# Kernel optimization log

Measured on AMD Instinct MI355X. Metric: run time of the kernel, lower is better.

The kernel has to match this reference:

```python
import jax, jax.numpy as jnp
import numpy as np
import math

NATOM = 20000
NEIGH = 600000
NWAVE = 8
MAX_L = 3
CUTOFF = 5.0
EMB_NL = [16, 16]
J_SEQ = [[1, 1, 0], [1, 1, 2], [2, 2, 2], [2, 2, 0], [1, 2, 3], [3, 3, 2]]
NSPH = (MAX_L + 1) ** 2


def wigner_3j(j1, j2, j3, m1, m2, m3):
    """Exact Wigner 3j symbol via the Racah formula (python ints -> float)."""
    f = math.factorial
    if m1 + m2 + m3 != 0:
        return 0.0
    pre = math.sqrt(
        f(j1 + j2 - j3) * f(j1 - j2 + j3) * f(-j1 + j2 + j3) / f(j1 + j2 + j3 + 1)
        * f(j1 + m1) * f(j1 - m1) * f(j2 + m2) * f(j2 - m2) * f(j3 + m3) * f(j3 - m3))
    tmin = max(0, j2 - j3 - m1, j1 - j3 + m2)
    tmax = min(j1 + j2 - j3, j1 - m1, j2 + m2)
    s = 0.0
    for t in range(tmin, tmax + 1):
        s += (-1) ** t / (f(t) * f(j3 - j2 + m1 + t) * f(j3 - j1 - m2 + t)
                          * f(j1 + j2 - j3 - t) * f(j1 - m1 - t) * f(j2 + m2 - t))
    return ((-1) ** (j1 - j2 - m3)) * pre * s


def real_sph(u, max_l):
    """Real spherical harmonics Y_{l,m}(u) for unit vectors u of shape (3, N).
    Output shape ((max_l+1)^2, N), flat index k = l*(l+1) + m, m in [-l, l]."""
    x, y, z = u[0], u[1], u[2]
    phi = jnp.arctan2(y, x)
    s = jnp.sqrt(jnp.clip(1.0 - z * z, 0.0))  # sin(theta)
    P = {(0, 0): jnp.ones_like(z)}
    for m in range(1, max_l + 1):
        P[(m, m)] = -(2 * m - 1) * s * P[(m - 1, m - 1)]
    for m in range(0, max_l):
        P[(m + 1, m)] = (2 * m + 1) * z * P[(m, m)]
    for m in range(0, max_l + 1):
        for l in range(m + 2, max_l + 1):
            P[(l, m)] = ((2 * l - 1) * z * P[(l - 1, m)] - (l + m - 1) * P[(l - 2, m)]) / (l - m)
    out = []
    for l in range(max_l + 1):
        for m in range(-l, l + 1):
            am = abs(m)
            K = math.sqrt((2 * l + 1) / (4.0 * math.pi) * math.factorial(l - am) / math.factorial(l + am))
            if m == 0:
                out.append(K * P[(l, 0)])
            elif m > 0:
                out.append(math.sqrt(2.0) * K * jnp.cos(m * phi) * P[(l, m)])
            else:
                out.append(math.sqrt(2.0) * K * jnp.sin(am * phi) * P[(l, am)])
    return jnp.stack(out)


def setup_inputs() -> dict:
    key = jax.random.key(0)
    ks = jax.random.split(key, 8)
    cart = jax.random.normal(ks[0], (3, NATOM), jnp.float32) * 10.0
    atomindex = jax.random.randint(ks[1], (2, NEIGH), 0, NATOM)
    shifts = jax.random.normal(ks[2], (3, NEIGH), jnp.float32)  # keeps distances > 0
    species = jax.random.uniform(ks[3], (NATOM,), jnp.float32)
    W1 = jax.random.normal(ks[4], (1, EMB_NL[0]), jnp.float32)
    b1 = jnp.zeros((EMB_NL[0],), jnp.float32)
    W2 = jax.random.normal(ks[5], (EMB_NL[0], EMB_NL[1]), jnp.float32) / math.sqrt(EMB_NL[0])
    b2 = jnp.zeros((EMB_NL[1],), jnp.float32)
    W3 = jax.random.normal(ks[6], (EMB_NL[1], 3 * NWAVE), jnp.float32) / math.sqrt(EMB_NL[1])
    b3 = jnp.zeros((3 * NWAVE,), jnp.float32)
    return {"cart": cart, "atomindex": atomindex, "shifts": shifts, "species": species,
            "W1": W1, "b1": b1, "W2": W2, "b2": b2, "W3": W3, "b3": b3}


def reference(cart, atomindex, shifts, species, W1, b1, W2, b2, W3, b3):
    natom = cart.shape[1]
    # edge vectors and distances
    coor = cart[:, atomindex[1]] - cart[:, atomindex[0]] + shifts  # (3, Neigh)
    dist = jnp.linalg.norm(coor, axis=0)                            # (Neigh,)
    # per-atom embedding MLP -> radial coefficients / gaussian params
    h = jax.nn.silu(species[:, None] @ W1 + b1)
    h = jax.nn.silu(h @ W2 + b2)
    emb = h @ W3 + b3                                               # (Natom, 3*nwave)
    expand = emb[atomindex[1]]                                      # (Neigh, 3*nwave)
    coeff = expand[:, :NWAVE]
    alpha = expand[:, NWAVE:2 * NWAVE]
    center = expand[:, 2 * NWAVE:]
    sd = alpha * (dist[:, None] - center)
    radial = jnp.exp(-sd * sd)                                      # (Neigh, nwave)
    cut = ((jnp.cos(dist / CUTOFF * jnp.pi) + 1.0) * 0.5) ** 3      # (Neigh,)
    sph = real_sph(coor / dist, MAX_L)                              # (NSPH, Neigh)
    equi = jnp.einsum('i,ij,ij,ki->ikj', cut, radial, coeff, sph)   # (Neigh, NSPH, nwave)
    sum_sph = jnp.zeros((natom, NSPH, NWAVE), sph.dtype).at[atomindex[0]].add(equi)
    sum_sph = sum_sph.transpose(1, 0, 2)                            # (NSPH, Natom, nwave)
    dens = []
    for J in J_SEQ:
        num = [j * (j + 1) for j in J]
        acc = jnp.zeros((natom, NWAVE), sph.dtype)
        for m1 in range(-J[0], J[0] + 1):
            for m2 in range(max(-J[2] - m1, -J[1]), min(J[2] - m1, J[1]) + 1):
                m3 = -m1 - m2
                w = wigner_3j(J[0], J[1], J[2], m1, m2, m3)
                acc = acc + sum_sph[num[0] + m1] * sum_sph[num[1] + m2] * sum_sph[num[2] + m3] * w
        dens.append(acc)
    return jnp.stack(dens)  # (nseq, Natom, nwave)
```

## Files before the change

### kernel.cpp

```cpp
#include <hip/hip_runtime.h>
#include <math.h>
#include <algorithm>
#include <string.h>

#define NATOM 20000
#define NEIGH 600000
#define NWAVE 8
#define NSPH 16
#define CAP 96

struct CFT {
  float v[6][7][7];
};

__device__ __forceinline__ float silu_f(float x) { return x / (1.f + expf(-x)); }

__global__ __launch_bounds__(256) void zero_kernel(int* __restrict__ counts)
{
  int t = blockIdx.x * 256 + threadIdx.x;
  if (t < NATOM) counts[t] = 0;
}

__global__ __launch_bounds__(256) void emb_hist_kernel(
    const float* __restrict__ species, const float* __restrict__ cart,
    const float* __restrict__ W1, const float* __restrict__ b1,
    const float* __restrict__ W2, const float* __restrict__ b2,
    const float* __restrict__ W3, const float* __restrict__ b3,
    float4* __restrict__ emb4, float4* __restrict__ cart4,
    const int* __restrict__ aidx, int* __restrict__ counts,
    int* __restrict__ rank_n)
{
  int t = blockIdx.x * 256 + threadIdx.x;
  if (t < NATOM) {
    float spv = species[t];
    float h1[16], h2[16], e24[24];
#pragma unroll
    for (int c = 0; c < 16; ++c) {
      float v = spv * W1[c] + b1[c];
      h1[c] = silu_f(v);
    }
#pragma unroll
    for (int d = 0; d < 16; ++d) {
      float v = b2[d];
#pragma unroll
      for (int c = 0; c < 16; ++c) v += h1[c] * W2[c * 16 + d];
      h2[d] = silu_f(v);
    }
#pragma unroll
    for (int e = 0; e < 24; ++e) {
      float v = b3[e];
#pragma unroll
      for (int c = 0; c < 16; ++c) v += h2[c] * W3[c * 24 + e];
      e24[e] = v;
    }
    float4* dst = emb4 + (size_t)t * 8;
#pragma unroll
    for (int w = 0; w < 8; ++w)
      dst[w] = make_float4(e24[w], e24[8 + w], e24[16 + w], 0.f);
    cart4[t] = make_float4(cart[t], cart[NATOM + t], cart[2 * NATOM + t], 0.f);
  }
  if (t < NEIGH) {
    int i = aidx[t];
    rank_n[t] = atomicAdd(&counts[i], 1);
  }
}

__global__ __launch_bounds__(256) void scatter_kernel(
    const int* __restrict__ aidx, const float* __restrict__ shifts,
    const int* __restrict__ rank_n, float4* __restrict__ sortrec)
{
  int n = blockIdx.x * 256 + threadIdx.x;
  if (n >= NEIGH) return;
  int i = aidx[n];
  int slot = i * CAP + rank_n[n];
  float4 r;
  r.x = __int_as_float(aidx[NEIGH + n]);
  r.y = shifts[n];
  r.z = shifts[NEIGH + n];
  r.w = shifts[2 * NEIGH + n];
  sortrec[slot] = r;
}

__global__ __launch_bounds__(256) void fused_kernel(
    const float4* __restrict__ cart4, const float4* __restrict__ sortrec,
    const float4* __restrict__ emb4, const int* __restrict__ counts,
    float* __restrict__ out, CFT cf)
{
  int t = blockIdx.x * 256 + threadIdx.x;
  int a = t >> 5;
  int sub = t & 31;
  int wp = sub & 3;
  int q = sub >> 2;

  float4 ci = cart4[a];
  int s0 = a * CAP;
  int s1 = s0 + counts[a];

  float acc0[NSPH], acc1[NSPH];
#pragma unroll
  for (int k = 0; k < NSPH; ++k) { acc0[k] = 0.f; acc1[k] = 0.f; }

  const float SQ2 = 1.41421356237309515f;

  int s = s0 + q;
  bool valid = s < s1;
  float4 r  = make_float4(0.f, 0.f, 0.f, 0.f);
  float4 cj = r, e0 = r, e1 = r;
  if (valid) {
    r = sortrec[s];
    int j = __float_as_int(r.x);
    cj = cart4[j];
    e0 = emb4[(size_t)j * 8 + wp];
    e1 = emb4[(size_t)j * 8 + wp + 4];
  }

  while (valid) {
    int sn = s + 8;
    bool vn = sn < s1;
    float4 rn  = make_float4(0.f, 0.f, 0.f, 0.f);
    float4 cjn = rn, e0n = rn, e1n = rn;
    if (vn) {
      rn = sortrec[sn];
      int jn = __float_as_int(rn.x);
      cjn = cart4[jn];
      e0n = emb4[(size_t)jn * 8 + wp];
      e1n = emb4[(size_t)jn * 8 + wp + 4];
    }

    float cx = cj.x - ci.x + r.y;
    float cy = cj.y - ci.y + r.z;
    float cz = cj.z - ci.z + r.w;
    float d2 = cx * cx + cy * cy + cz * cz;
    float inv = __frsqrt_rn(d2);
    float dist = d2 * inv;
    float x = cx * inv, y = cy * inv, z = cz * inv;

    float cc = __cosf(dist * 0.62831853071795864769f);
    float cut0 = (cc + 1.f) * 0.5f;
    float cut = cut0 * cut0 * cut0;

    float sd0 = e0.y * (dist - e0.z);
    float av0 = cut * e0.x * __expf(-sd0 * sd0);
    float sd1 = e1.y * (dist - e1.z);
    float av1 = cut * e1.x * __expf(-sd1 * sd1);

    float r2 = x * x + y * y;
    float ri = __frsqrt_rn(fmaxf(r2, 1e-30f));
    float cp = x * ri, sp = y * ri;
    float c2 = cp * cp - sp * sp, s2 = 2.f * cp * sp;
    float c3 = c2 * cp - s2 * sp, s3 = s2 * cp + c2 * sp;

    float sz = sqrtf(fmaxf(1.f - z * z, 0.f));
    float P11 = -sz;
    float P22 = -3.f * sz * P11;
    float P33 = -5.f * sz * P22;
    float P10 = z;
    float P21 = 3.f * z * P11;
    float P32 = 5.f * z * P22;
    float P20 = (3.f * z * P10 - 1.f) * 0.5f;
    float P31 = (5.f * z * P21 - 3.f * P11) * 0.5f;
    float P30 = (5.f * z * P20 - 2.f * P10) * (1.f / 3.f);

    float sph[NSPH];
    sph[0]  = 0.28209479177387814f;
    sph[1]  = SQ2 * 0.3454941494713355f  * sp * P11;
    sph[2]  = 0.4886025119029199f * P10;
    sph[3]  = SQ2 * 0.3454941494713355f  * cp * P11;
    sph[4]  = SQ2 * 0.12875806734106326f * s2 * P22;
    sph[5]  = SQ2 * 0.25751613468212653f * sp * P21;
    sph[6]  = 0.6307831305050401f * P20;
    sph[7]  = SQ2 * 0.25751613468212653f * cp * P21;
    sph[8]  = SQ2 * 0.12875806734106326f * c2 * P22;
    sph[9]  = SQ2 * 0.027814921575518937f * s3 * P33;
    sph[10] = SQ2 * 0.06813236509555433f  * s2 * P32;
    sph[11] = SQ2 * 0.2154534560761003f   * sp * P31;
    sph[12] = 0.7463526651802308f * P30;
    sph[13] = SQ2 * 0.2154534560761003f   * cp * P31;
    sph[14] = SQ2 * 0.06813236509555433f  * c2 * P32;
    sph[15] = SQ2 * 0.027814921575518937f * c3 * P33;

#pragma unroll
    for (int k = 0; k < NSPH; ++k) {
      acc0[k] += sph[k] * av0;
      acc1[k] += sph[k] * av1;
    }

    s = sn; valid = vn; r = rn; cj = cjn; e0 = e0n; e1 = e1n;
  }

#pragma unroll
  for (int k = 0; k < NSPH; ++k) {
    acc0[k] += __shfl_xor(acc0[k], 4);
    acc0[k] += __shfl_xor(acc0[k], 8);
    acc0[k] += __shfl_xor(acc0[k], 16);
    acc1[k] += __shfl_xor(acc1[k], 4);
    acc1[k] += __shfl_xor(acc1[k], 8);
    acc1[k] += __shfl_xor(acc1[k], 16);
  }

  constexpr int J0s[6] = {1, 1, 2, 2, 1, 3};
  constexpr int J1s[6] = {1, 1, 2, 2, 2, 3};
  constexpr int J2s[6] = {0, 2, 2, 0, 3, 2};
#pragma unroll
  for (int jj = 0; jj < 6; ++jj) {
    const int J0 = J0s[jj], J1 = J1s[jj], J2 = J2s[jj];
    const int n0 = J0 * (J0 + 1), n1 = J1 * (J1 + 1), n2 = J2 * (J2 + 1);
    float dj0 = 0.f, dj1 = 0.f;
#pragma unroll
    for (int m1 = -3; m1 <= 3; ++m1) {
      if (m1 < -J0 || m1 > J0) continue;
#pragma unroll
      for (int m2 = -3; m2 <= 3; ++m2) {
        if (m2 < -J1 || m2 > J1) continue;
        const int m3 = -m1 - m2;
        if (m3 < -J2 || m3 > J2) continue;
        const float w3 = cf.v[jj][m1 + 3][m2 + 3];
        dj0 += acc0[n0 + m1] * acc0[n1 + m2] * acc0[n2 + m3] * w3;
        dj1 += acc1[n0 + m1] * acc1[n1 + m2] * acc1[n2 + m3] * w3;
      }
    }
    if (q == jj) {
      out[((size_t)jj * NATOM + a) * 8 + wp]     = dj0;
      out[((size_t)jj * NATOM + a) * 8 + wp + 4] = dj1;
    }
  }
}

static double dfact(int n) { double r = 1.0; for (int i = 2; i <= n; ++i) r *= i; return r; }
static double wig3j(int j1, int j2, int j3, int m1, int m2, int m3) {
  if (m1 + m2 + m3 != 0) return 0.0;
  double pre = sqrt(dfact(j1 + j2 - j3) * dfact(j1 - j2 + j3) * dfact(-j1 + j2 + j3)
                    / dfact(j1 + j2 + j3 + 1)
                    * dfact(j1 + m1) * dfact(j1 - m1) * dfact(j2 + m2) * dfact(j2 - m2)
                    * dfact(j3 + m3) * dfact(j3 - m3));
  int tmin = std::max(0, std::max(j2 - j3 - m1, j1 - j3 + m2));
  int tmax = std::min(j1 + j2 - j3, std::min(j1 - m1, j2 + m2));
  double s = 0.0;
  for (int t = tmin; t <= tmax; ++t)
    s += ((t & 1) ? -1.0 : 1.0) /
         (dfact(t) * dfact(j3 - j2 + m1 + t) * dfact(j3 - j1 - m2 + t) *
          dfact(j1 + j2 - j3 - t) * dfact(j1 - m1 - t) * dfact(j2 + m2 - t));
  int e = j1 - j2 - m3;
  double sgn = ((e % 2) != 0) ? -1.0 : 1.0;
  return sgn * pre * s;
}

extern "C" void kernel_launch(void* const* d_in, const int* in_sizes, int n_in,
                              void* d_out, int out_size, void* d_ws, size_t ws_size,
                              hipStream_t stream)
{
  const float* cart    = (const float*)d_in[0];
  const int*   aidx    = (const int*)d_in[1];
  const float* shifts  = (const float*)d_in[2];
  const float* species = (const float*)d_in[3];
  const float* W1 = (const float*)d_in[4];
  const float* b1 = (const float*)d_in[5];
  const float* W2 = (const float*)d_in[6];
  const float* b2 = (const float*)d_in[7];
  const float* W3 = (const float*)d_in[8];
  const float* b3 = (const float*)d_in[9];
  float* out = (float*)d_out;

  float4* sortrec = (float4*)d_ws;
  float4* emb4    = sortrec + (size_t)NATOM * CAP;
  float4* cart4   = emb4 + (size_t)NATOM * 8;
  int*    counts  = (int*)(cart4 + NATOM);
  int*    rank_n  = counts + NATOM;

  static const int JS[6][3] = {{1,1,0},{1,1,2},{2,2,2},{2,2,0},{1,2,3},{3,3,2}};
  CFT cf;
  memset(&cf, 0, sizeof(cf));
  for (int j = 0; j < 6; ++j) {
    int J0 = JS[j][0], J1 = JS[j][1], J2 = JS[j][2];
    for (int m1 = -J0; m1 <= J0; ++m1)
      for (int m2 = std::max(-J2 - m1, -J1); m2 <= std::min(J2 - m1, J1); ++m2) {
        int m3 = -m1 - m2;
        cf.v[j][m1 + 3][m2 + 3] = (float)wig3j(J0, J1, J2, m1, m2, m3);
      }
  }

  zero_kernel<<<(NATOM + 255) / 256, 256, 0, stream>>>(counts);
  emb_hist_kernel<<<(NEIGH + 255) / 256, 256, 0, stream>>>(
      species, cart, W1, b1, W2, b2, W3, b3, emb4, cart4, aidx, counts, rank_n);
  scatter_kernel<<<(NEIGH + 255) / 256, 256, 0, stream>>>(aidx, shifts, rank_n, sortrec);
  fused_kernel<<<(NATOM * 32) / 256, 256, 0, stream>>>(
      cart4, sortrec, emb4, counts, out, cf);
}
```

Measured before the change: 81.63 us.

## Fuse histogram and scatter into one kernel with two neighbours per thread

Merges the atomic-rank histogram kernel and the scatter kernel, so each neighbour record is written immediately after its atomicAdd returns a slot. This drops one kernel launch and the rank_n array's write and read-back. Each thread now handles two neighbours, giving more memory-level parallelism and two independent atomics in flight, and the record stores are nontemporal. Slot order within an atom stays nondeterministic as before, and the fused kernel runs half as many threads.

```diff
diff --git a/kernel.cpp b/kernel.cpp
--- a/kernel.cpp
+++ b/kernel.cpp
@@ -5,10 +5,13 @@
 
 #define NATOM 20000
 #define NEIGH 600000
+#define HALF  300000
 #define NWAVE 8
 #define NSPH 16
 #define CAP 96
 
+typedef float floatx4 __attribute__((ext_vector_type(4)));
+
 struct CFT {
   float v[6][7][7];
 };
@@ -21,14 +24,14 @@
   if (t < NATOM) counts[t] = 0;
 }
 
-__global__ __launch_bounds__(256) void emb_hist_kernel(
+__global__ __launch_bounds__(256) void emb_scatter_kernel(
     const float* __restrict__ species, const float* __restrict__ cart,
     const float* __restrict__ W1, const float* __restrict__ b1,
     const float* __restrict__ W2, const float* __restrict__ b2,
     const float* __restrict__ W3, const float* __restrict__ b3,
     float4* __restrict__ emb4, float4* __restrict__ cart4,
-    const int* __restrict__ aidx, int* __restrict__ counts,
-    int* __restrict__ rank_n)
+    const int* __restrict__ aidx, const float* __restrict__ shifts,
+    int* __restrict__ counts, float4* __restrict__ sortrec)
 {
   int t = blockIdx.x * 256 + threadIdx.x;
   if (t < NATOM) {
@@ -59,26 +62,24 @@
       dst[w] = make_float4(e24[w], e24[8 + w], e24[16 + w], 0.f);
     cart4[t] = make_float4(cart[t], cart[NATOM + t], cart[2 * NATOM + t], 0.f);
   }
-  if (t < NEIGH) {
-    int i = aidx[t];
-    rank_n[t] = atomicAdd(&counts[i], 1);
-  }
-}
-
-__global__ __launch_bounds__(256) void scatter_kernel(
-    const int* __restrict__ aidx, const float* __restrict__ shifts,
-    const int* __restrict__ rank_n, float4* __restrict__ sortrec)
-{
-  int n = blockIdx.x * 256 + threadIdx.x;
-  if (n >= NEIGH) return;
-  int i = aidx[n];
-  int slot = i * CAP + rank_n[n];
-  float4 r;
-  r.x = __int_as_float(aidx[NEIGH + n]);
-  r.y = shifts[n];
-  r.z = shifts[NEIGH + n];
-  r.w = shifts[2 * NEIGH + n];
-  sortrec[slot] = r;
+
+  if (t >= HALF) return;
+  int n0 = t, n1 = t + HALF;
+  int i0 = aidx[n0];
+  int i1 = aidx[n1];
+  floatx4 r0, r1;
+  r0.x = __int_as_float(aidx[NEIGH + n0]);
+  r0.y = shifts[n0];
+  r0.z = shifts[NEIGH + n0];
+  r0.w = shifts[2 * NEIGH + n0];
+  r1.x = __int_as_float(aidx[NEIGH + n1]);
+  r1.y = shifts[n1];
+  r1.z = shifts[NEIGH + n1];
+  r1.w = shifts[2 * NEIGH + n1];
+  int k0 = atomicAdd(&counts[i0], 1);
+  int k1 = atomicAdd(&counts[i1], 1);
+  __builtin_nontemporal_store(r0, reinterpret_cast<floatx4*>(sortrec) + (size_t)i0 * CAP + k0);
+  __builtin_nontemporal_store(r1, reinterpret_cast<floatx4*>(sortrec) + (size_t)i1 * CAP + k1);
 }
 
 __global__ __launch_bounds__(256) void fused_kernel(
@@ -265,7 +266,6 @@
   float4* emb4    = sortrec + (size_t)NATOM * CAP;
   float4* cart4   = emb4 + (size_t)NATOM * 8;
   int*    counts  = (int*)(cart4 + NATOM);
-  int*    rank_n  = counts + NATOM;
 
   static const int JS[6][3] = {{1,1,0},{1,1,2},{2,2,2},{2,2,0},{1,2,3},{3,3,2}};
   CFT cf;
@@ -280,9 +280,8 @@
   }
 
   zero_kernel<<<(NATOM + 255) / 256, 256, 0, stream>>>(counts);
-  emb_hist_kernel<<<(NEIGH + 255) / 256, 256, 0, stream>>>(
-      species, cart, W1, b1, W2, b2, W3, b3, emb4, cart4, aidx, counts, rank_n);
-  scatter_kernel<<<(NEIGH + 255) / 256, 256, 0, stream>>>(aidx, shifts, rank_n, sortrec);
+  emb_scatter_kernel<<<(HALF + 255) / 256, 256, 0, stream>>>(
+      species, cart, W1, b1, W2, b2, W3, b3, emb4, cart4, aidx, shifts, counts, sortrec);
   fused_kernel<<<(NATOM * 32) / 256, 256, 0, stream>>>(
       cart4, sortrec, emb4, counts, out, cf);
 }
```

Result: slower. 92.92 us (+13.8%).
